# Optimization experiments

Measured on AMD Instinct MI355X. Metric: run time of the kernel, lower is better.

Reference implementation:

```python
import jax, jax.numpy as jnp
import numpy as np

D_MODEL = 1024
NUM_HEADS = 16
D_HEAD = D_MODEL // NUM_HEADS


def _rope(x):
    """Rotary embedding, lucidrains interleaved convention, applied along axis -2.

    x: (..., n, d). Positions are arange(n); freq_i = 10000**(-2i/d), each freq
    repeated twice (interleaved); rotate_half swaps adjacent pairs (-x2, x1).
    """
    n, d = x.shape[-2], x.shape[-1]
    inv_freq = 1.0 / (10000.0 ** (jnp.arange(0, d, 2, dtype=jnp.float32) / d))  # (d/2,)
    freqs = jnp.arange(n, dtype=jnp.float32)[:, None] * inv_freq[None, :]       # (n, d/2)
    emb = jnp.repeat(freqs, 2, axis=-1)                                         # (n, d)
    cos, sin = jnp.cos(emb).astype(x.dtype), jnp.sin(emb).astype(x.dtype)
    xp = x.reshape(x.shape[:-1] + (d // 2, 2))
    rot = jnp.stack([-xp[..., 1], xp[..., 0]], axis=-1).reshape(x.shape)
    return x * cos + rot * sin


def setup_inputs() -> dict:
    key = jax.random.key(0)
    ks = jax.random.split(key, 11)
    B, S = 4, 2048
    mk = lambda k, shape: (jax.random.normal(k, shape, dtype=jnp.float32) * 0.02)
    return {
        "query": jax.random.normal(ks[0], (B, S, D_MODEL), dtype=jnp.float32),
        "key": jax.random.normal(ks[1], (B, S, D_MODEL), dtype=jnp.float32),
        "value": jax.random.normal(ks[2], (B, S, D_MODEL), dtype=jnp.float32),
        "Wq": mk(ks[3], (D_MODEL, D_MODEL)), "bq": jnp.zeros((D_MODEL,), jnp.float32),
        "Wk": mk(ks[4], (D_MODEL, D_MODEL)), "bk": jnp.zeros((D_MODEL,), jnp.float32),
        "Wv": mk(ks[5], (D_MODEL, D_MODEL)), "bv": jnp.zeros((D_MODEL,), jnp.float32),
        "Wo": mk(ks[6], (D_MODEL, D_MODEL)), "bo": jnp.zeros((D_MODEL,), jnp.float32),
    }


def reference(query, key, value, Wq, bq, Wk, bk, Wv, bv, Wo, bo):
    B, S, _ = query.shape
    H, dh = NUM_HEADS, D_HEAD
    # projections (torch Linear: x @ W.T + b)
    q = (query @ Wq.T + bq).reshape(B, S, H, dh)           # (b, t, h, d)
    k = (key @ Wk.T + bk).reshape(B, S, H, dh).transpose(0, 2, 1, 3)   # (b, h, t, d)
    v = (value @ Wv.T + bv).reshape(B, S, H, dh).transpose(0, 2, 1, 3)  # (b, h, t, d)
    # Faithful to source: query rotated along axis -2 = HEADS axis (pre-permute),
    # key rotated along axis -2 = time axis.
    q = _rope(q)                                            # positions over heads (source quirk)
    k = _rope(k)                                            # positions over time
    q = q.transpose(0, 2, 1, 3)                             # (b, h, t, d)
    scores = jnp.einsum("bhqd,bhkd->bhqk", q, k) / jnp.sqrt(jnp.float32(D_MODEL))
    attn = jax.nn.softmax(scores, axis=-1)
    ctx = jnp.einsum("bhqk,bhkd->bhqd", attn, v)            # (b, h, t, d)
    ctx = ctx.transpose(0, 2, 1, 3).reshape(B, S, H * dh)   # (b, t, d_model)
    return ctx @ Wo.T + bo
```

## Files before the change

### kernel.cpp

```cpp
#include <hip/hip_runtime.h>

using u16 = unsigned short;
typedef __bf16 bf16x8 __attribute__((ext_vector_type(8)));
typedef __bf16 bf16x2 __attribute__((ext_vector_type(2)));
typedef float f32x4 __attribute__((ext_vector_type(4)));

#if __has_builtin(__builtin_amdgcn_exp2f)
#define QSCALE 0.04508422468443852f
#define FEXP(x) __builtin_amdgcn_exp2f(x)
#else
#define QSCALE 0.03125f
#define FEXP(x) __expf(x)
#endif

__device__ __forceinline__ u16 f2bf(float f) {
  unsigned u = __builtin_bit_cast(unsigned, f);
  u += 0x7FFFu + ((u >> 16) & 1u);
  return (u16)(u >> 16);
}

#define GLD_LDS16(g, l)                                                                   \
  __builtin_amdgcn_global_load_lds((const __attribute__((address_space(1))) void*)(g),    \
                                   (__attribute__((address_space(3))) void*)(l), 16, 0, 0)

template <int LOG2NB>
__global__ void cvt_multi(const float* __restrict__ i0, const float* __restrict__ i1,
                          const float* __restrict__ i2, const float* __restrict__ i3,
                          u16* __restrict__ o0, u16* __restrict__ o1, u16* __restrict__ o2,
                          u16* __restrict__ o3, int n4) {
  const int which = blockIdx.x >> LOG2NB;
  const float* in = which == 0 ? i0 : which == 1 ? i1 : which == 2 ? i2 : i3;
  u16* out = which == 0 ? o0 : which == 1 ? o1 : which == 2 ? o2 : o3;
  int i = (blockIdx.x & ((1 << LOG2NB) - 1)) * blockDim.x + threadIdx.x;
  const int st = (1 << LOG2NB) * blockDim.x;
  for (; i < n4; i += st) {
    float4 v = reinterpret_cast<const float4*>(in)[i];
    ushort4 o = make_ushort4(f2bf(v.x), f2bf(v.y), f2bf(v.z), f2bf(v.w));
    reinterpret_cast<ushort4*>(out)[i] = o;
  }
}

template <int EPI>
__global__ __launch_bounds__(512, 4) void gemm_bt(const u16* __restrict__ A,
                                                  const u16* __restrict__ Bt,
                                                  const float* __restrict__ bias,
                                                  void* __restrict__ outp) {
  __shared__ u16 lA[3][128 * 32];
  __shared__ u16 lB[3][128 * 32];
  const int tid = threadIdx.x;
  const int l = tid & 63, w = tid >> 6;
  const int wr = w >> 2, wc = w & 3;
  const int l15 = l & 15, lg = l >> 4;
  const int rsw = (l15 >> 1) & 3;
  const int bid = ((blockIdx.x & 7) << 6) | (blockIdx.x >> 3);
  const int br = bid >> 3, bc = bid & 7;

  f32x4 acc[4][2];
#pragma unroll
  for (int m = 0; m < 4; ++m)
#pragma unroll
    for (int n = 0; n < 2; ++n) acc[m][n] = f32x4{0.f, 0.f, 0.f, 0.f};

  const int srow = tid >> 2;
  const int gch = (tid & 3) ^ ((tid >> 3) & 3);
  const u16* Abase = A + (size_t)(br * 128 + srow) * 1024 + gch * 8;
  const u16* Bbase = Bt + (size_t)(bc * 128 + srow) * 1024 + gch * 8;

  auto stage = [&](int buf, int kk) {
    GLD_LDS16(Abase + kk, &lA[buf][tid * 8]);
    GLD_LDS16(Bbase + kk, &lB[buf][tid * 8]);
  };

  auto compute = [&](int cur) {
    const int c = ((lg ^ rsw) << 3);
    bf16x8 af[4], bfr[2];
#pragma unroll
    for (int m = 0; m < 4; ++m)
      af[m] = *reinterpret_cast<const bf16x8*>(&lA[cur][(wr * 64 + m * 16 + l15) * 32 + c]);
#pragma unroll
    for (int n = 0; n < 2; ++n)
      bfr[n] = *reinterpret_cast<const bf16x8*>(&lB[cur][(wc * 32 + n * 16 + l15) * 32 + c]);
#pragma unroll
    for (int m = 0; m < 4; ++m)
#pragma unroll
      for (int n = 0; n < 2; ++n)
        acc[m][n] = __builtin_amdgcn_mfma_f32_16x16x32_bf16(af[m], bfr[n], acc[m][n], 0, 0, 0);
  };

  stage(0, 0);
  stage(1, 32);
  asm volatile("s_waitcnt vmcnt(2)" ::: "memory");
  __builtin_amdgcn_s_barrier();
  __builtin_amdgcn_sched_barrier(0);

  int cur = 0, nx2 = 2;
  for (int it = 0; it < 31; ++it) {
    if (it < 30) stage(nx2, (it + 2) * 32);
    compute(cur);
    if (it < 30)
      asm volatile("s_waitcnt vmcnt(2)" ::: "memory");
    else
      asm volatile("s_waitcnt vmcnt(0)" ::: "memory");
    __builtin_amdgcn_s_barrier();
    __builtin_amdgcn_sched_barrier(0);
    cur = cur == 2 ? 0 : cur + 1;
    nx2 = nx2 == 2 ? 0 : nx2 + 1;
  }
  compute(cur);

  const int row0 = br * 128 + wr * 64;
  const int col0 = bc * 128 + wc * 32;

  if constexpr (EPI == 0 || EPI == 1) {
    u16* out = reinterpret_cast<u16*>(outp);
#pragma unroll
    for (int n = 0; n < 2; ++n) {
      const int gn = col0 + n * 16 + l15;
      const float bv2 = bias[gn];
      const int p = (gn & 63) >> 1;
      const float invf = __expf((float)p * -0.28782313663f);
      float ss = 0.f, cc = 0.f;
      if constexpr (EPI == 0) {
        const float th = (float)(gn >> 6) * invf;
        sincosf(th, &ss, &cc);
      }
#pragma unroll
      for (int m = 0; m < 4; ++m) {
        const int gm0 = row0 + m * 16 + lg * 4;
#pragma unroll
        for (int r = 0; r < 4; ++r) {
          float x = acc[m][n][r] + bv2;
          if constexpr (EPI == 1) {
            const float th = (float)((gm0 + r) & 2047) * invf;
            sincosf(th, &ss, &cc);
          }
          const float xp = __shfl_xor(x, 1);
          float o = (gn & 1) ? fmaf(xp, ss, x * cc) : fmaf(-xp, ss, x * cc);
          if constexpr (EPI == 0) o *= QSCALE;
          out[(size_t)(gm0 + r) * 1024 + gn] = f2bf(o);
        }
      }
    }
  } else if constexpr (EPI == 2) {
    u16* vT = reinterpret_cast<u16*>(outp);
#pragma unroll
    for (int n = 0; n < 2; ++n) {
      const int gn = col0 + n * 16 + l15;
      const float bv2 = bias[gn];
      const int hh = gn >> 6, dd = gn & 63;
#pragma unroll
      for (int m = 0; m < 4; ++m) {
        const int gm0 = row0 + m * 16 + lg * 4;
        const int bb = gm0 >> 11, s0 = gm0 & 2047;
        ushort4 pk = make_ushort4(f2bf(acc[m][n][0] + bv2), f2bf(acc[m][n][1] + bv2),
                                  f2bf(acc[m][n][2] + bv2), f2bf(acc[m][n][3] + bv2));
        *reinterpret_cast<ushort4*>(vT + ((size_t)((bb * 16 + hh) * 64 + dd) * 2048 + s0)) = pk;
      }
    }
  } else {
    float* out = reinterpret_cast<float*>(outp);
#pragma unroll
    for (int n = 0; n < 2; ++n) {
      const int gn = col0 + n * 16 + l15;
      const float bv2 = bias[gn];
#pragma unroll
      for (int m = 0; m < 4; ++m) {
        const int gm0 = row0 + m * 16 + lg * 4;
#pragma unroll
        for (int r = 0; r < 4; ++r) out[(size_t)(gm0 + r) * 1024 + gn] = acc[m][n][r] + bv2;
      }
    }
  }
}

__global__ __launch_bounds__(512, 6) void attn_fwd(const u16* __restrict__ Q,
                                                   const u16* __restrict__ K,
                                                   const u16* __restrict__ Vt,
                                                   u16* __restrict__ ctx) {
  __shared__ u16 sK[3][64 * 64];
  __shared__ u16 sV[3][64 * 64];
  const int tid = threadIdx.x;
  const int l = tid & 63, w = tid >> 6;
  const int l15 = l & 15, lg = l >> 4;
  const int swz = (l15 & 7) << 3;
  const int wgid = ((blockIdx.x & 7) << 7) | (blockIdx.x >> 3);
  const int qt = wgid & 15, bh = wgid >> 4;
  const int b = bh >> 4, h = bh & 15;

  bf16x8 qf0, qf1;
  {
    const u16* qp = Q + (size_t)(b * 2048 + qt * 128 + w * 16 + l15) * 1024 + h * 64 + lg * 8;
    qf0 = *reinterpret_cast<const bf16x8*>(qp);
    qf1 = *reinterpret_cast<const bf16x8*>(qp + 32);
  }

  bf16x8 ones;
#pragma unroll
  for (int i = 0; i < 8; ++i) ones[i] = (__bf16)1.0f;

  f32x4 acc_l = f32x4{0.f, 0.f, 0.f, 0.f};
  f32x4 acc_o[4];
#pragma unroll
  for (int n = 0; n < 4; ++n) acc_o[n] = f32x4{0.f, 0.f, 0.f, 0.f};

  const int srow = tid >> 3;
  const int scol = ((tid & 7) ^ (srow & 7)) * 8;
  const int krow = (srow & 0x23) | ((srow & 0x0C) << 1) | ((srow & 0x10) >> 2);
  const u16* Kbase = K + (size_t)(b * 2048 + krow) * 1024 + h * 64 + scol;
  const u16* Vbase = Vt + (size_t)(bh * 64 + srow) * 2048 + scol;

  auto stage = [&](int buf, int j) {
    GLD_LDS16(Kbase + (size_t)(j * 64) * 1024, &sK[buf][tid * 8]);
    GLD_LDS16(Vbase + j * 64, &sV[buf][tid * 8]);
  };

  stage(0, 0);
  stage(1, 1);
  asm volatile("s_waitcnt vmcnt(2)" ::: "memory");
  __builtin_amdgcn_s_barrier();
  __builtin_amdgcn_sched_barrier(0);

  int cur = 0, nx2 = 2;
  for (int j = 0; j < 32; ++j) {
    if (j < 30) stage(nx2, j + 2);

    f32x4 accs[4];
#pragma unroll
    for (int nk = 0; nk < 4; ++nk) accs[nk] = f32x4{0.f, 0.f, 0.f, 0.f};
    const int c0 = (lg * 8) ^ swz;
    __builtin_amdgcn_s_setprio(1);
#pragma unroll
    for (int nk = 0; nk < 4; ++nk) {
      bf16x8 kf0 = *reinterpret_cast<const bf16x8*>(&sK[cur][(nk * 16 + l15) * 64 + c0]);
      bf16x8 kf1 = *reinterpret_cast<const bf16x8*>(&sK[cur][(nk * 16 + l15) * 64 + (c0 ^ 32)]);
      accs[nk] = __builtin_amdgcn_mfma_f32_16x16x32_bf16(kf0, qf0, accs[nk], 0, 0, 0);
      accs[nk] = __builtin_amdgcn_mfma_f32_16x16x32_bf16(kf1, qf1, accs[nk], 0, 0, 0);
    }
    __builtin_amdgcn_s_setprio(0);

    unsigned wpk[4][2];
#pragma unroll
    for (int nk = 0; nk < 4; ++nk) {
      const float p0 = FEXP(accs[nk][0]), p1 = FEXP(accs[nk][1]);
      const float p2 = FEXP(accs[nk][2]), p3 = FEXP(accs[nk][3]);
      bf16x2 t0, t1;
      t0.x = (__bf16)p0; t0.y = (__bf16)p1;
      t1.x = (__bf16)p2; t1.y = (__bf16)p3;
      wpk[nk][0] = __builtin_bit_cast(unsigned, t0);
      wpk[nk][1] = __builtin_bit_cast(unsigned, t1);
    }

    __builtin_amdgcn_s_setprio(1);
#pragma unroll
    for (int ks = 0; ks < 2; ++ks) {
      const uint4 paw = make_uint4(wpk[2 * ks][0], wpk[2 * ks][1],
                                   wpk[2 * ks + 1][0], wpk[2 * ks + 1][1]);
      const bf16x8 pa = __builtin_bit_cast(bf16x8, paw);
      acc_l = __builtin_amdgcn_mfma_f32_16x16x32_bf16(ones, pa, acc_l, 0, 0, 0);
#pragma unroll
      for (int n = 0; n < 4; ++n) {
        bf16x8 vf = *reinterpret_cast<const bf16x8*>(
            &sV[cur][(n * 16 + l15) * 64 + ((ks * 32 + lg * 8) ^ swz)]);
        acc_o[n] = __builtin_amdgcn_mfma_f32_16x16x32_bf16(vf, pa, acc_o[n], 0, 0, 0);
      }
    }
    __builtin_amdgcn_s_setprio(0);

    if (j < 31) {
      if (j < 30)
        asm volatile("s_waitcnt vmcnt(2)" ::: "memory");
      else
        asm volatile("s_waitcnt vmcnt(0)" ::: "memory");
      __builtin_amdgcn_s_barrier();
      __builtin_amdgcn_sched_barrier(0);
    }
    cur = cur == 2 ? 0 : cur + 1;
    nx2 = nx2 == 2 ? 0 : nx2 + 1;
  }

  const float inv = 1.f / acc_l[0];
  u16* obase = ctx + (size_t)(b * 2048 + qt * 128 + w * 16 + l15) * 1024 + h * 64;
#pragma unroll
  for (int n = 0; n < 4; ++n) {
    ushort4 pk = make_ushort4(f2bf(acc_o[n][0] * inv), f2bf(acc_o[n][1] * inv),
                              f2bf(acc_o[n][2] * inv), f2bf(acc_o[n][3] * inv));
    *reinterpret_cast<ushort4*>(obase + n * 16 + lg * 4) = pk;
  }
}

extern "C" void kernel_launch(void* const* d_in, const int* in_sizes, int n_in, void* d_out,
                              int out_size, void* d_ws, size_t ws_size, hipStream_t stream) {
  (void)in_sizes; (void)n_in; (void)out_size; (void)ws_size;
  const float* query = (const float*)d_in[0];
  const float* key = (const float*)d_in[1];
  const float* value = (const float*)d_in[2];
  const float* Wq = (const float*)d_in[3];
  const float* bq = (const float*)d_in[4];
  const float* Wk = (const float*)d_in[5];
  const float* bk = (const float*)d_in[6];
  const float* Wv = (const float*)d_in[7];
  const float* bv = (const float*)d_in[8];
  const float* Wo = (const float*)d_in[9];
  const float* bo = (const float*)d_in[10];

  char* ws = (char*)d_ws;
  const size_t MB = (size_t)1 << 20;
  u16* xq = (u16*)(ws + 0 * MB);
  u16* xk = (u16*)(ws + 16 * MB);
  u16* xv = (u16*)(ws + 32 * MB);
  u16* wqb = (u16*)(ws + 48 * MB);
  u16* wkb = (u16*)(ws + 50 * MB);
  u16* wvb = (u16*)(ws + 52 * MB);
  u16* wob = (u16*)(ws + 54 * MB);
  u16* qb = (u16*)(ws + 56 * MB);
  u16* kb = (u16*)(ws + 72 * MB);
  u16* vT = (u16*)(ws + 88 * MB);
  u16* cx = (u16*)(ws + 104 * MB);

  cvt_multi<9><<<1536, 256, 0, stream>>>(query, key, value, query, xq, xk, xv, xq, 2097152);
  cvt_multi<6><<<256, 256, 0, stream>>>(Wq, Wk, Wv, Wo, wqb, wkb, wvb, wob, 262144);

  gemm_bt<0><<<512, 512, 0, stream>>>(xq, wqb, bq, qb);
  gemm_bt<1><<<512, 512, 0, stream>>>(xk, wkb, bk, kb);
  gemm_bt<2><<<512, 512, 0, stream>>>(xv, wvb, bv, vT);
  attn_fwd<<<1024, 512, 0, stream>>>(qb, kb, vT, cx);
  gemm_bt<3><<<512, 512, 0, stream>>>(cx, wob, bo, (float*)d_out);
}
```

Measured before the change: 218.3 us.

## Widen GEMM k-tile to 64 with double buffering; give attention two query groups per wave

The projection GEMMs now stage 64-wide k slices into two LDS buffers, with a new XOR swizzle and a full wait each iteration, instead of 32-wide slices in a triple buffer. The aim is to halve the number of barriers and loop iterations. The attention kernel gives each wave 32 query rows (two 16-row groups) that share every K/V tile loaded into LDS, and halves the grid to 512 blocks with a lower occupancy bound. This is meant to halve K/V global and LDS traffic per query, at the cost of more registers, fewer resident waves and less overlap from the shallower GEMM pipeline.

```diff
diff --git a/kernel.cpp b/kernel.cpp
--- a/kernel.cpp
+++ b/kernel.cpp
@@ -45,13 +45,12 @@
                                                   const u16* __restrict__ Bt,
                                                   const float* __restrict__ bias,
                                                   void* __restrict__ outp) {
-  __shared__ u16 lA[3][128 * 32];
-  __shared__ u16 lB[3][128 * 32];
+  __shared__ u16 lA[2][128 * 64];
+  __shared__ u16 lB[2][128 * 64];
   const int tid = threadIdx.x;
   const int l = tid & 63, w = tid >> 6;
   const int wr = w >> 2, wc = w & 3;
   const int l15 = l & 15, lg = l >> 4;
-  const int rsw = (l15 >> 1) & 3;
   const int bid = ((blockIdx.x & 7) << 6) | (blockIdx.x >> 3);
   const int br = bid >> 3, bc = bid & 7;
 
@@ -61,52 +60,52 @@
 #pragma unroll
     for (int n = 0; n < 2; ++n) acc[m][n] = f32x4{0.f, 0.f, 0.f, 0.f};
 
-  const int srow = tid >> 2;
-  const int gch = (tid & 3) ^ ((tid >> 3) & 3);
+  const int srow = tid >> 3;
+  const int gch = (tid & 7) ^ (srow & 7);
   const u16* Abase = A + (size_t)(br * 128 + srow) * 1024 + gch * 8;
   const u16* Bbase = Bt + (size_t)(bc * 128 + srow) * 1024 + gch * 8;
 
   auto stage = [&](int buf, int kk) {
     GLD_LDS16(Abase + kk, &lA[buf][tid * 8]);
+    GLD_LDS16(Abase + (size_t)64 * 1024 + kk, &lA[buf][4096 + tid * 8]);
     GLD_LDS16(Bbase + kk, &lB[buf][tid * 8]);
+    GLD_LDS16(Bbase + (size_t)64 * 1024 + kk, &lB[buf][4096 + tid * 8]);
   };
 
   auto compute = [&](int cur) {
-    const int c = ((lg ^ rsw) << 3);
-    bf16x8 af[4], bfr[2];
-#pragma unroll
-    for (int m = 0; m < 4; ++m)
-      af[m] = *reinterpret_cast<const bf16x8*>(&lA[cur][(wr * 64 + m * 16 + l15) * 32 + c]);
-#pragma unroll
-    for (int n = 0; n < 2; ++n)
-      bfr[n] = *reinterpret_cast<const bf16x8*>(&lB[cur][(wc * 32 + n * 16 + l15) * 32 + c]);
-#pragma unroll
-    for (int m = 0; m < 4; ++m)
+#pragma unroll
+    for (int ks = 0; ks < 2; ++ks) {
+      const int c = (((ks * 4 + lg) ^ (l15 & 7)) << 3);
+      bf16x8 af[4], bfr[2];
+#pragma unroll
+      for (int m = 0; m < 4; ++m)
+        af[m] = *reinterpret_cast<const bf16x8*>(&lA[cur][(wr * 64 + m * 16 + l15) * 64 + c]);
 #pragma unroll
       for (int n = 0; n < 2; ++n)
-        acc[m][n] = __builtin_amdgcn_mfma_f32_16x16x32_bf16(af[m], bfr[n], acc[m][n], 0, 0, 0);
+        bfr[n] = *reinterpret_cast<const bf16x8*>(&lB[cur][(wc * 32 + n * 16 + l15) * 64 + c]);
+#pragma unroll
+      for (int m = 0; m < 4; ++m)
+#pragma unroll
+        for (int n = 0; n < 2; ++n)
+          acc[m][n] = __builtin_amdgcn_mfma_f32_16x16x32_bf16(af[m], bfr[n], acc[m][n], 0, 0, 0);
+    }
   };
 
   stage(0, 0);
-  stage(1, 32);
-  asm volatile("s_waitcnt vmcnt(2)" ::: "memory");
+  asm volatile("s_waitcnt vmcnt(0)" ::: "memory");
   __builtin_amdgcn_s_barrier();
   __builtin_amdgcn_sched_barrier(0);
 
-  int cur = 0, nx2 = 2;
-  for (int it = 0; it < 31; ++it) {
-    if (it < 30) stage(nx2, (it + 2) * 32);
+  for (int it = 0; it < 16; ++it) {
+    const int cur = it & 1;
+    if (it < 15) stage(cur ^ 1, (it + 1) * 64);
     compute(cur);
-    if (it < 30)
-      asm volatile("s_waitcnt vmcnt(2)" ::: "memory");
-    else
+    if (it < 15) {
       asm volatile("s_waitcnt vmcnt(0)" ::: "memory");
-    __builtin_amdgcn_s_barrier();
-    __builtin_amdgcn_sched_barrier(0);
-    cur = cur == 2 ? 0 : cur + 1;
-    nx2 = nx2 == 2 ? 0 : nx2 + 1;
-  }
-  compute(cur);
+      __builtin_amdgcn_s_barrier();
+      __builtin_amdgcn_sched_barrier(0);
+    }
+  }
 
   const int row0 = br * 128 + wr * 64;
   const int col0 = bc * 128 + wc * 32;
@@ -173,7 +172,7 @@
   }
 }
 
-__global__ __launch_bounds__(512, 6) void attn_fwd(const u16* __restrict__ Q,
+__global__ __launch_bounds__(512, 4) void attn_fwd(const u16* __restrict__ Q,
                                                    const u16* __restrict__ K,
                                                    const u16* __restrict__ Vt,
                                                    u16* __restrict__ ctx) {
@@ -183,25 +182,31 @@
   const int l = tid & 63, w = tid >> 6;
   const int l15 = l & 15, lg = l >> 4;
   const int swz = (l15 & 7) << 3;
-  const int wgid = ((blockIdx.x & 7) << 7) | (blockIdx.x >> 3);
-  const int qt = wgid & 15, bh = wgid >> 4;
+  const int wgid = ((blockIdx.x & 7) << 6) | (blockIdx.x >> 3);
+  const int qt = wgid & 7, bh = wgid >> 3;
   const int b = bh >> 4, h = bh & 15;
 
-  bf16x8 qf0, qf1;
-  {
-    const u16* qp = Q + (size_t)(b * 2048 + qt * 128 + w * 16 + l15) * 1024 + h * 64 + lg * 8;
-    qf0 = *reinterpret_cast<const bf16x8*>(qp);
-    qf1 = *reinterpret_cast<const bf16x8*>(qp + 32);
+  bf16x8 qf[2][2];
+#pragma unroll
+  for (int g = 0; g < 2; ++g) {
+    const u16* qp =
+        Q + (size_t)(b * 2048 + qt * 256 + w * 32 + g * 16 + l15) * 1024 + h * 64 + lg * 8;
+    qf[g][0] = *reinterpret_cast<const bf16x8*>(qp);
+    qf[g][1] = *reinterpret_cast<const bf16x8*>(qp + 32);
   }
 
   bf16x8 ones;
 #pragma unroll
   for (int i = 0; i < 8; ++i) ones[i] = (__bf16)1.0f;
 
-  f32x4 acc_l = f32x4{0.f, 0.f, 0.f, 0.f};
-  f32x4 acc_o[4];
-#pragma unroll
-  for (int n = 0; n < 4; ++n) acc_o[n] = f32x4{0.f, 0.f, 0.f, 0.f};
+  f32x4 acc_l[2];
+  f32x4 acc_o[2][4];
+#pragma unroll
+  for (int g = 0; g < 2; ++g) {
+    acc_l[g] = f32x4{0.f, 0.f, 0.f, 0.f};
+#pragma unroll
+    for (int n = 0; n < 4; ++n) acc_o[g][n] = f32x4{0.f, 0.f, 0.f, 0.f};
+  }
 
   const int srow = tid >> 3;
   const int scol = ((tid & 7) ^ (srow & 7)) * 8;
@@ -224,44 +229,49 @@
   for (int j = 0; j < 32; ++j) {
     if (j < 30) stage(nx2, j + 2);
 
-    f32x4 accs[4];
-#pragma unroll
-    for (int nk = 0; nk < 4; ++nk) accs[nk] = f32x4{0.f, 0.f, 0.f, 0.f};
     const int c0 = (lg * 8) ^ swz;
+    unsigned wpk[2][4][2];
+#pragma unroll
+    for (int g = 0; g < 2; ++g) {
+      f32x4 accs[4];
+#pragma unroll
+      for (int nk = 0; nk < 4; ++nk) accs[nk] = f32x4{0.f, 0.f, 0.f, 0.f};
+      __builtin_amdgcn_s_setprio(1);
+#pragma unroll
+      for (int nk = 0; nk < 4; ++nk) {
+        bf16x8 kf0 = *reinterpret_cast<const bf16x8*>(&sK[cur][(nk * 16 + l15) * 64 + c0]);
+        bf16x8 kf1 = *reinterpret_cast<const bf16x8*>(&sK[cur][(nk * 16 + l15) * 64 + (c0 ^ 32)]);
+        accs[nk] = __builtin_amdgcn_mfma_f32_16x16x32_bf16(kf0, qf[g][0], accs[nk], 0, 0, 0);
+        accs[nk] = __builtin_amdgcn_mfma_f32_16x16x32_bf16(kf1, qf[g][1], accs[nk], 0, 0, 0);
+      }
+      __builtin_amdgcn_s_setprio(0);
+#pragma unroll
+      for (int nk = 0; nk < 4; ++nk) {
+        const float p0 = FEXP(accs[nk][0]), p1 = FEXP(accs[nk][1]);
+        const float p2 = FEXP(accs[nk][2]), p3 = FEXP(accs[nk][3]);
+        bf16x2 t0, t1;
+        t0.x = (__bf16)p0; t0.y = (__bf16)p1;
+        t1.x = (__bf16)p2; t1.y = (__bf16)p3;
+        wpk[g][nk][0] = __builtin_bit_cast(unsigned, t0);
+        wpk[g][nk][1] = __builtin_bit_cast(unsigned, t1);
+      }
+    }
+
     __builtin_amdgcn_s_setprio(1);
 #pragma unroll
-    for (int nk = 0; nk < 4; ++nk) {
-      bf16x8 kf0 = *reinterpret_cast<const bf16x8*>(&sK[cur][(nk * 16 + l15) * 64 + c0]);
-      bf16x8 kf1 = *reinterpret_cast<const bf16x8*>(&sK[cur][(nk * 16 + l15) * 64 + (c0 ^ 32)]);
-      accs[nk] = __builtin_amdgcn_mfma_f32_16x16x32_bf16(kf0, qf0, accs[nk], 0, 0, 0);
-      accs[nk] = __builtin_amdgcn_mfma_f32_16x16x32_bf16(kf1, qf1, accs[nk], 0, 0, 0);
-    }
-    __builtin_amdgcn_s_setprio(0);
-
-    unsigned wpk[4][2];
-#pragma unroll
-    for (int nk = 0; nk < 4; ++nk) {
-      const float p0 = FEXP(accs[nk][0]), p1 = FEXP(accs[nk][1]);
-      const float p2 = FEXP(accs[nk][2]), p3 = FEXP(accs[nk][3]);
-      bf16x2 t0, t1;
-      t0.x = (__bf16)p0; t0.y = (__bf16)p1;
-      t1.x = (__bf16)p2; t1.y = (__bf16)p3;
-      wpk[nk][0] = __builtin_bit_cast(unsigned, t0);
-      wpk[nk][1] = __builtin_bit_cast(unsigned, t1);
-    }
-
-    __builtin_amdgcn_s_setprio(1);
-#pragma unroll
-    for (int ks = 0; ks < 2; ++ks) {
-      const uint4 paw = make_uint4(wpk[2 * ks][0], wpk[2 * ks][1],
-                                   wpk[2 * ks + 1][0], wpk[2 * ks + 1][1]);
-      const bf16x8 pa = __builtin_bit_cast(bf16x8, paw);
-      acc_l = __builtin_amdgcn_mfma_f32_16x16x32_bf16(ones, pa, acc_l, 0, 0, 0);
-#pragma unroll
-      for (int n = 0; n < 4; ++n) {
-        bf16x8 vf = *reinterpret_cast<const bf16x8*>(
-            &sV[cur][(n * 16 + l15) * 64 + ((ks * 32 + lg * 8) ^ swz)]);
-        acc_o[n] = __builtin_amdgcn_mfma_f32_16x16x32_bf16(vf, pa, acc_o[n], 0, 0, 0);
+    for (int g = 0; g < 2; ++g) {
+#pragma unroll
+      for (int ks = 0; ks < 2; ++ks) {
+        const uint4 paw = make_uint4(wpk[g][2 * ks][0], wpk[g][2 * ks][1],
+                                     wpk[g][2 * ks + 1][0], wpk[g][2 * ks + 1][1]);
+        const bf16x8 pa = __builtin_bit_cast(bf16x8, paw);
+        acc_l[g] = __builtin_amdgcn_mfma_f32_16x16x32_bf16(ones, pa, acc_l[g], 0, 0, 0);
+#pragma unroll
+        for (int n = 0; n < 4; ++n) {
+          bf16x8 vf = *reinterpret_cast<const bf16x8*>(
+              &sV[cur][(n * 16 + l15) * 64 + ((ks * 32 + lg * 8) ^ swz)]);
+          acc_o[g][n] = __builtin_amdgcn_mfma_f32_16x16x32_bf16(vf, pa, acc_o[g][n], 0, 0, 0);
+        }
       }
     }
     __builtin_amdgcn_s_setprio(0);
@@ -278,13 +288,17 @@
     nx2 = nx2 == 2 ? 0 : nx2 + 1;
   }
 
-  const float inv = 1.f / acc_l[0];
-  u16* obase = ctx + (size_t)(b * 2048 + qt * 128 + w * 16 + l15) * 1024 + h * 64;
-#pragma unroll
-  for (int n = 0; n < 4; ++n) {
-    ushort4 pk = make_ushort4(f2bf(acc_o[n][0] * inv), f2bf(acc_o[n][1] * inv),
-                              f2bf(acc_o[n][2] * inv), f2bf(acc_o[n][3] * inv));
-    *reinterpret_cast<ushort4*>(obase + n * 16 + lg * 4) = pk;
+#pragma unroll
+  for (int g = 0; g < 2; ++g) {
+    const float inv = 1.f / acc_l[g][0];
+    u16* obase =
+        ctx + (size_t)(b * 2048 + qt * 256 + w * 32 + g * 16 + l15) * 1024 + h * 64;
+#pragma unroll
+    for (int n = 0; n < 4; ++n) {
+      ushort4 pk = make_ushort4(f2bf(acc_o[g][n][0] * inv), f2bf(acc_o[g][n][1] * inv),
+                                f2bf(acc_o[g][n][2] * inv), f2bf(acc_o[g][n][3] * inv));
+      *reinterpret_cast<ushort4*>(obase + n * 16 + lg * 4) = pk;
+    }
   }
 }
 
@@ -323,6 +337,6 @@
   gemm_bt<0><<<512, 512, 0, stream>>>(xq, wqb, bq, qb);
   gemm_bt<1><<<512, 512, 0, stream>>>(xk, wkb, bk, kb);
   gemm_bt<2><<<512, 512, 0, stream>>>(xv, wvb, bv, vT);
-  attn_fwd<<<1024, 512, 0, stream>>>(qb, kb, vT, cx);
+  attn_fwd<<<512, 512, 0, stream>>>(qb, kb, vT, cx);
   gemm_bt<3><<<512, 512, 0, stream>>>(cx, wob, bo, (float*)d_out);
 }
```

Result: faster. 195.8 us (-10.3%).
